# Kernel optimization log

Measured on AMD Instinct MI355X. Metric: run time of the kernel, lower is better.

The kernel has to match this reference:

```python
import jax, jax.numpy as jnp
import numpy as np

TS = 16      # tile size
ST = 4       # stride
IN = 224     # image size
G = (IN - TS) // ST + 1   # 53 tiles per side
L = G * G                 # 2809 tiles
CH = [3 * L, 3 * L // 4, 3 * L // 16, 3 * L // 4, 3 * L]  # [8427,2106,526,2106,8427]

# torch_dct-style unnormalized DCT-II matrix and its exact inverse (DCT-III based)
_n = np.arange(TS)
_k = np.arange(TS)[:, None]
_C = np.cos(np.pi * (2 * _n[None, :] + 1) * _k / (2 * TS))  # [k, n]
D_DCT = jnp.asarray(2.0 * _C, jnp.float32)                   # dct: y = D @ x
_w = np.ones(TS); _w[0] = 0.5
D_IDCT = jnp.asarray((_C.T * _w[None, :]) / TS, jnp.float32) # idct: x = Dinv @ y

# gather/scatter indices for unfold/fold (constants)
IH = (np.arange(G) * ST)[:, None] + np.arange(TS)[None, :]   # [G, TS]
IW = IH


def setup_inputs() -> dict:
    key = jax.random.key(0)
    ks = jax.random.split(key, 9)
    x = jax.random.normal(ks[0], (8, 3, IN, IN), jnp.float32)
    def lin(k, o, c):
        return jax.random.normal(k, (o, c), jnp.float32) * 0.02
    return {
        'x': x,
        'w1': lin(ks[1], CH[1], CH[0]), 'b1': jnp.zeros((CH[1],), jnp.float32),
        'w2': lin(ks[2], CH[2], CH[1]), 'b2': jnp.zeros((CH[2],), jnp.float32),
        'w3': lin(ks[3], CH[3], CH[2]), 'b3': jnp.zeros((CH[3],), jnp.float32),
        'w4': lin(ks[4], CH[4], CH[3]), 'b4': jnp.zeros((CH[4],), jnp.float32),
    }


def _forward(x, w1, b1, w2, b2, w3, b3, w4, b4):
    b = x.shape[0]
    # unfold: gather overlapping 16x16 patches -> [b, 3, G, G, TS, TS]
    p = x[:, :, IH[:, None, :, None], IW[None, :, None, :]]
    # torch ordering after permute+reshape: channel index = l*3 + c
    tiles = p.transpose(0, 2, 3, 1, 4, 5).reshape(b, 3 * L, TS, TS)
    # 2D DCT (unnormalized DCT-II along last two dims)
    dct_tiles = jnp.einsum('km,ln,bcmn->bckl', D_DCT, D_DCT, tiles)
    # mask net: stack of 1x1 convs over the tile-channel dim
    h = dct_tiles / (TS * TS)
    h = jax.nn.relu(jnp.einsum('oc,bchw->bohw', w1, h) + b1[:, None, None])
    h = jax.nn.relu(jnp.einsum('oc,bchw->bohw', w2, h) + b2[:, None, None])
    h = jax.nn.relu(jnp.einsum('oc,bchw->bohw', w3, h) + b3[:, None, None])
    masks = jax.nn.sigmoid(jnp.einsum('oc,bchw->bohw', w4, h) + b4[:, None, None])
    clean_dct = masks * dct_tiles
    # 2D inverse DCT
    clean_tiles = jnp.einsum('mk,nl,bckl->bcmn', D_IDCT, D_IDCT, clean_dct)
    # fold: scatter-add patches back with overlap
    ct = clean_tiles.reshape(b, G, G, 3, TS, TS).transpose(0, 3, 1, 2, 4, 5)
    out = jnp.zeros((b, 3, IN, IN), x.dtype)
    out = out.at[:, :, IH[:, None, :, None], IW[None, :, None, :]].add(ct)
    # scale = fold(unfold(ones)): per-pixel overlap counts (recomputed per call, as in source)
    scale = jnp.zeros((IN, IN), x.dtype)
    scale = scale.at[IH[:, None, :, None], IW[None, :, None, :]].add(
        jnp.ones((G, G, TS, TS), x.dtype))
    return out / scale


def reference(x, w1, b1, w2, b2, w3, b3, w4, b4):
    return _forward(x, w1, b1, w2, b2, w3, b3, w4, b4)
```

## Files before the change

### kernel.cpp

```cpp
#include <hip/hip_runtime.h>
#include <stdint.h>

constexpr int INSZ = 224;
constexpr int GD   = 53;
constexpr int C0R = 8427, C1R = 2106, C2R = 526;
constexpr int C0P = 8448, C1P = 2304, C2P = 640;
constexpr int NTOK = 2048;

typedef __attribute__((ext_vector_type(4))) float f32x4;
typedef __attribute__((ext_vector_type(8))) short bf16x8;

constexpr float CT[64] = {
  1.00000000f,  0.99518473f,  0.98078528f,  0.95694034f,
  0.92387953f,  0.88192126f,  0.83146961f,  0.77301045f,
  0.70710678f,  0.63439328f,  0.55557023f,  0.47139674f,
  0.38268343f,  0.29028468f,  0.19509032f,  0.09801714f,
  0.00000000f, -0.09801714f, -0.19509032f, -0.29028468f,
 -0.38268343f, -0.47139674f, -0.55557023f, -0.63439328f,
 -0.70710678f, -0.77301045f, -0.83146961f, -0.88192126f,
 -0.92387953f, -0.95694034f, -0.98078528f, -0.99518473f,
 -1.00000000f, -0.99518473f, -0.98078528f, -0.95694034f,
 -0.92387953f, -0.88192126f, -0.83146961f, -0.77301045f,
 -0.70710678f, -0.63439328f, -0.55557023f, -0.47139674f,
 -0.38268343f, -0.29028468f, -0.19509032f, -0.09801714f,
 -0.00000000f,  0.09801714f,  0.19509032f,  0.29028468f,
  0.38268343f,  0.47139674f,  0.55557023f,  0.63439328f,
  0.70710678f,  0.77301045f,  0.83146961f,  0.88192126f,
  0.92387953f,  0.95694034f,  0.98078528f,  0.99518473f
};
constexpr float Dfwd(int k, int n) { return 2.0f * CT[((2 * n + 1) * k) & 63]; }
constexpr float Dinv(int n, int k) { return CT[((2 * n + 1) * k) & 63] * (k == 0 ? 0.03125f : 0.0625f); }

constexpr int TRS_R = 20, TRS_T = 336;
constexpr int TRS_SZ = 15 * TRS_T + 15 * TRS_R + 16;

__device__ __forceinline__ unsigned short f2bf(float f) {
  union { float f; unsigned u; } v; v.f = f;
  return (unsigned short)((v.u + 0x7FFFu + ((v.u >> 16) & 1u)) >> 16);
}
__device__ __forceinline__ float bf2f(unsigned short b) {
  union { unsigned u; float f; } v; v.u = ((unsigned)b) << 16;
  return v.f;
}

__device__ __forceinline__ void gload_lds16(const void* g, void* l) {
  __builtin_amdgcn_global_load_lds(
      (__attribute__((address_space(1))) unsigned int*)(uintptr_t)g,
      (__attribute__((address_space(3))) unsigned int*)(unsigned int)(uintptr_t)l,
      16, 0, 0);
}

__device__ __forceinline__ void xcd_tile(int& bx, int& by) {
  const int gx = gridDim.x, gy = gridDim.y;
  const int nwg = gx * gy;
  const int bid = blockIdx.y * gx + blockIdx.x;
  const int cpx = nwg >> 3;
  const int l = (bid & 7) * cpx + (bid >> 3);
  const int stripe = gy << 2;
  const int bxg = l / stripe;
  const int r = l - bxg * stripe;
  const int rem = gx - (bxg << 2);
  const int w = rem < 4 ? rem : 4;
  by = r / w;
  bx = (bxg << 2) + (r - by * w);
}

constexpr int CV1_GPR = C0P / 8;
constexpr int CV1_TOT = C1P * CV1_GPR;
__global__ __launch_bounds__(256)
void cvt_pad8_w1(const float* __restrict__ src, unsigned short* __restrict__ dst) {
  const int i = blockIdx.x * 256 + threadIdx.x;
  if (i >= CV1_TOT) return;
  const int m = i / CV1_GPR;
  const int k0 = (i - m * CV1_GPR) * 8;
  const float* sr = src + (size_t)m * C0R + k0;
  const bool mok = (m < C1R);
  unsigned short h[8];
#pragma unroll
  for (int e = 0; e < 8; ++e)
    h[e] = f2bf((mok && k0 + e < C0R) ? sr[e] : 0.f);
  uint4 pk;
  pk.x = (unsigned)h[0] | ((unsigned)h[1] << 16);
  pk.y = (unsigned)h[2] | ((unsigned)h[3] << 16);
  pk.z = (unsigned)h[4] | ((unsigned)h[5] << 16);
  pk.w = (unsigned)h[6] | ((unsigned)h[7] << 16);
  *(uint4*)&dst[(size_t)m * C0P + k0] = pk;
}

constexpr int CV8_1 = C2P * C1P / 8;
constexpr int CV8_2 = CV8_1 + C1P * C2P / 8;
constexpr int CV8_T = CV8_2 + C0P * C1P / 8;
__global__ __launch_bounds__(256)
void cvt_pad8_all(const float* __restrict__ w2, const float* __restrict__ w3,
                  const float* __restrict__ w4, unsigned short* __restrict__ d2,
                  unsigned short* __restrict__ d3, unsigned short* __restrict__ d4) {
  const int i = blockIdx.x * 256 + threadIdx.x;
  const float* src; unsigned short* dst;
  int m, k0, Kreal, Mreal, Kp;
  if (i < CV8_1) {
    const int gpr = C1P / 8;
    m = i / gpr; k0 = (i - m * gpr) * 8;
    src = w2; dst = d2; Mreal = C2R; Kreal = C1R; Kp = C1P;
  } else if (i < CV8_2) {
    const int j = i - CV8_1;
    const int gpr = C2P / 8;
    m = j / gpr; k0 = (j - m * gpr) * 8;
    src = w3; dst = d3; Mreal = C1R; Kreal = C2R; Kp = C2P;
  } else {
    const int j = i - CV8_2;
    const int gpr = C1P / 8;
    m = j / gpr; k0 = (j - m * gpr) * 8;
    src = w4; dst = d4; Mreal = C0R; Kreal = C1R; Kp = C1P;
  }
  const float* sr = src + (size_t)m * Kreal + k0;
  const bool mok = (m < Mreal);
  unsigned short h[8];
#pragma unroll
  for (int e = 0; e < 8; ++e)
    h[e] = f2bf((mok && k0 + e < Kreal) ? sr[e] : 0.f);
  uint4 pk;
  pk.x = (unsigned)h[0] | ((unsigned)h[1] << 16);
  pk.y = (unsigned)h[2] | ((unsigned)h[3] << 16);
  pk.z = (unsigned)h[4] | ((unsigned)h[5] << 16);
  pk.w = (unsigned)h[6] | ((unsigned)h[7] << 16);
  *(uint4*)&dst[(size_t)m * Kp + k0] = pk;
}

__global__ __launch_bounds__(256)
void dct_h0(const float* __restrict__ x, unsigned short* __restrict__ H0) {
  __shared__ float trp[TRS_SZ];
  __shared__ unsigned short hst[256 * 64];
  const int tid = threadIdx.x;
  const int b   = blockIdx.y;
  const int c0  = blockIdx.x * 64;
  const int t = tid >> 4, q = tid & 15;

  for (int g = 0; g < 4; ++g) {
    const int c = c0 + g * 16 + t;
    float p[16];
    {
      float4 v0{}, v1{}, v2{}, v3{};
      if (c < C0R) {
        const int ch = c % 3, gw = (c / 3) % GD, gh = c / (3 * GD);
        const float* xr = x + ((size_t)(b * 3 + ch) * INSZ + (gh * 4 + q)) * INSZ + gw * 4;
        v0 = *(const float4*)(xr);      v1 = *(const float4*)(xr + 4);
        v2 = *(const float4*)(xr + 8);  v3 = *(const float4*)(xr + 12);
      }
      p[0]=v0.x; p[1]=v0.y; p[2]=v0.z; p[3]=v0.w;
      p[4]=v1.x; p[5]=v1.y; p[6]=v1.z; p[7]=v1.w;
      p[8]=v2.x; p[9]=v2.y; p[10]=v2.z; p[11]=v2.w;
      p[12]=v3.x; p[13]=v3.y; p[14]=v3.z; p[15]=v3.w;
    }
    float r[16];
#pragma unroll
    for (int k = 0; k < 16; ++k) {
      float s = 0.f;
#pragma unroll
      for (int n = 0; n < 16; ++n) s += p[n] * Dfwd(k, n);
      r[k] = s;
    }
    float* wr = &trp[t * TRS_T + q * TRS_R];
#pragma unroll
    for (int k = 0; k < 16; k += 4)
      *(float4*)(wr + k) = make_float4(r[k], r[k+1], r[k+2], r[k+3]);
    __syncthreads();
    const int j = q;
    float rr[16];
#pragma unroll
    for (int i = 0; i < 16; ++i) rr[i] = trp[t * TRS_T + i * TRS_R + j];
#pragma unroll
    for (int k = 0; k < 16; ++k) {
      float s = 0.f;
#pragma unroll
      for (int i = 0; i < 16; ++i) s += rr[i] * Dfwd(k, i);
      hst[(k * 16 + j) * 64 + g * 16 + t] = f2bf(s * (1.f / 256.f));
    }
    __syncthreads();
  }
  const size_t base = ((size_t)b * 256) * C0P + c0;
#pragma unroll
  for (int i = 0; i < 8; ++i) {
    const int s = i * 256 + tid;
    const int kl = s >> 3, c16 = s & 7;
    *(uint4*)&H0[base + (size_t)kl * C0P + c16 * 8] = *(const uint4*)&hst[kl * 64 + c16 * 8];
  }
}

template<int ACT, int OUT_NM, int SPLITK>
__global__ __launch_bounds__(512, 2)
void gemm256(const unsigned short* __restrict__ W, const unsigned short* __restrict__ Ht,
             const float* __restrict__ bias, void* __restrict__ outp,
             int ldo, int Kp, int chunkK) {
  __shared__ unsigned short As[4][8192];
  __shared__ unsigned short Bs[4][8192];
  int bx, by; xcd_tile(bx, by);
  const int m0 = bx * 256, n0 = by * 256;
  const int tid = threadIdx.x;
  const int w = tid >> 6, lane = tid & 63;
  const int wr = w >> 2, wc = w & 3;
  const int lhi = lane >> 4, llo = lane & 15;
  const int kbase = SPLITK ? blockIdx.z * chunkK : 0;
  const int nkt = chunkK >> 5;

  const int srow = tid >> 2;
  const int slgc = ((tid & 3) ^ ((srow >> 1) & 3)) * 8;

  f32x4 acc[8][4];
#pragma unroll
  for (int i = 0; i < 8; ++i)
#pragma unroll
    for (int j = 0; j < 4; ++j) acc[i][j] = f32x4{0.f, 0.f, 0.f, 0.f};

  auto STAGE_A = [&](int kt, int buf) {
    const int kb = kbase + kt * 32 + slgc;
    gload_lds16(W + (size_t)(m0 + srow) * Kp + kb,       &As[buf][w * 512]);
    gload_lds16(W + (size_t)(m0 + 128 + srow) * Kp + kb, &As[buf][4096 + w * 512]);
  };
  auto STAGE_B = [&](int kt, int buf) {
    const int kb = kbase + kt * 32 + slgc;
    gload_lds16(Ht + (size_t)(n0 + srow) * Kp + kb,       &Bs[buf][w * 512]);
    gload_lds16(Ht + (size_t)(n0 + 128 + srow) * Kp + kb, &Bs[buf][4096 + w * 512]);
  };

  STAGE_A(0, 0); STAGE_B(0, 0);
  if (nkt > 1) { STAGE_A(1, 1); STAGE_B(1, 1); }
  if (nkt > 2) { STAGE_A(2, 2); STAGE_B(2, 2); }

  for (int kt = 0; kt < nkt; ++kt) {
    const int buf  = kt & 3;
    const int sbuf = (kt + 3) & 3;
    if (kt + 3 <= nkt)      asm volatile("s_waitcnt vmcnt(8)" ::: "memory");
    else if (kt + 2 == nkt) asm volatile("s_waitcnt vmcnt(4)" ::: "memory");
    else                    asm volatile("s_waitcnt vmcnt(0)" ::: "memory");
    __builtin_amdgcn_s_barrier();
    __builtin_amdgcn_sched_barrier(0);

    bf16x8 af[4], bfr[4];
#pragma unroll
    for (int mi = 0; mi < 4; ++mi) {
      const int row = wr * 128 + mi * 16 + llo;
      af[mi] = *(const bf16x8*)(&As[buf][row * 32 + ((lhi ^ ((row >> 1) & 3)) << 3)]);
    }
#pragma unroll
    for (int ni = 0; ni < 4; ++ni) {
      const int row = wc * 64 + ni * 16 + llo;
      bfr[ni] = *(const bf16x8*)(&Bs[buf][row * 32 + ((lhi ^ ((row >> 1) & 3)) << 3)]);
    }
    if (kt + 3 < nkt) STAGE_A(kt + 3, sbuf);
    __builtin_amdgcn_s_setprio(1);
#pragma unroll
    for (int mi = 0; mi < 4; ++mi)
#pragma unroll
      for (int ni = 0; ni < 4; ++ni)
        acc[mi][ni] = OUT_NM
          ? __builtin_amdgcn_mfma_f32_16x16x32_bf16(bfr[ni], af[mi], acc[mi][ni], 0, 0, 0)
          : __builtin_amdgcn_mfma_f32_16x16x32_bf16(af[mi], bfr[ni], acc[mi][ni], 0, 0, 0);
    __builtin_amdgcn_s_setprio(0);
#pragma unroll
    for (int mi = 0; mi < 4; ++mi) {
      const int row = wr * 128 + 64 + mi * 16 + llo;
      af[mi] = *(const bf16x8*)(&As[buf][row * 32 + ((lhi ^ ((row >> 1) & 3)) << 3)]);
    }
    if (kt + 3 < nkt) STAGE_B(kt + 3, sbuf);
    __builtin_amdgcn_s_setprio(1);
#pragma unroll
    for (int mi = 0; mi < 4; ++mi)
#pragma unroll
      for (int ni = 0; ni < 4; ++ni)
        acc[4 + mi][ni] = OUT_NM
          ? __builtin_amdgcn_mfma_f32_16x16x32_bf16(bfr[ni], af[mi], acc[4 + mi][ni], 0, 0, 0)
          : __builtin_amdgcn_mfma_f32_16x16x32_bf16(af[mi], bfr[ni], acc[4 + mi][ni], 0, 0, 0);
    __builtin_amdgcn_s_setprio(0);
  }

  if (SPLITK) {
    float* pz = (float*)outp + (size_t)blockIdx.z * ((size_t)NTOK * ldo);
#pragma unroll
    for (int mh = 0; mh < 2; ++mh)
#pragma unroll
      for (int mi = 0; mi < 4; ++mi) {
        const int mg = m0 + wr * 128 + mh * 64 + mi * 16 + llo;
#pragma unroll
        for (int ni = 0; ni < 4; ++ni) {
          const int ng = n0 + wc * 64 + ni * 16 + lhi * 4;
#pragma unroll
          for (int r = 0; r < 4; ++r)
            pz[(size_t)(ng + r) * ldo + mg] = acc[mh * 4 + mi][ni][r];
        }
      }
  } else {
    unsigned short* out = (unsigned short*)outp;
#pragma unroll
    for (int mh = 0; mh < 2; ++mh)
#pragma unroll
      for (int mi = 0; mi < 4; ++mi) {
        const int mgb = m0 + wr * 128 + mh * 64 + mi * 16 + lhi * 4;
#pragma unroll
        for (int ni = 0; ni < 4; ++ni) {
          const int ng = n0 + wc * 64 + ni * 16 + llo;
#pragma unroll
          for (int r = 0; r < 4; ++r) {
            const int mg = mgb + r;
            float v = acc[mh * 4 + mi][ni][r] + bias[mg];
            if (ACT == 1) v = fmaxf(v, 0.f);
            else if (ACT == 2) v = 1.f / (1.f + expf(-v));
            out[(size_t)mg * ldo + ng] = f2bf(v);
          }
        }
      }
  }
}

template<int OUT_NM>
__device__ __forceinline__ void gemm_core(
    const unsigned short* __restrict__ W, const unsigned short* __restrict__ Ht,
    unsigned short (*As)[128 * 32], unsigned short (*Bs)[128 * 32],
    int m0, int n0, int Kp, int kbase, int nkt, int w, int lane, f32x4 acc[4][4]) {
  const int wr = w >> 1, wc = w & 1;
  const int lhi = lane >> 4, llo = lane & 15;

  const int chunk0 = w * 64 + lane;
  const int row0 = chunk0 >> 2, kc0 = chunk0 & 3;
  const int kcg0 = kc0 ^ ((row0 >> 1) & 3);
  const int chunk1 = 256 + w * 64 + lane;
  const int row1 = chunk1 >> 2, kc1 = chunk1 & 3;
  const int kcg1 = kc1 ^ ((row1 >> 1) & 3);

  auto STAGE = [&](int kt, int sel) {
    const int kb = kbase + kt * 32;
    gload_lds16(W  + (size_t)(m0 + row0) * Kp + kb + kcg0 * 8, &As[sel][(w * 64) * 8]);
    gload_lds16(Ht + (size_t)(n0 + row0) * Kp + kb + kcg0 * 8, &Bs[sel][(w * 64) * 8]);
    gload_lds16(W  + (size_t)(m0 + row1) * Kp + kb + kcg1 * 8, &As[sel][(256 + w * 64) * 8]);
    gload_lds16(Ht + (size_t)(n0 + row1) * Kp + kb + kcg1 * 8, &Bs[sel][(256 + w * 64) * 8]);
  };

  STAGE(0, 0);
  if (nkt > 1) STAGE(1, 1);

  int cur = 0, nxt = 1, nx2 = 2;
  for (int kt = 0; kt < nkt; ++kt) {
    if (kt + 1 < nkt) {
      asm volatile("s_waitcnt vmcnt(4)" ::: "memory");
      __builtin_amdgcn_s_barrier();
      __builtin_amdgcn_sched_barrier(0);
      if (kt + 2 < nkt) STAGE(kt + 2, nx2);
    } else {
      asm volatile("s_waitcnt vmcnt(0)" ::: "memory");
      __builtin_amdgcn_s_barrier();
      __builtin_amdgcn_sched_barrier(0);
    }
    bf16x8 af[4], bfr[4];
#pragma unroll
    for (int mi = 0; mi < 4; ++mi) {
      const int row = wr * 64 + mi * 16 + llo;
      af[mi] = *(const bf16x8*)(&As[cur][row * 32 + (lhi ^ ((row >> 1) & 3)) * 8]);
    }
#pragma unroll
    for (int ni = 0; ni < 4; ++ni) {
      const int row = wc * 64 + ni * 16 + llo;
      bfr[ni] = *(const bf16x8*)(&Bs[cur][row * 32 + (lhi ^ ((row >> 1) & 3)) * 8]);
    }
#pragma unroll
    for (int mi = 0; mi < 4; ++mi)
#pragma unroll
      for (int ni = 0; ni < 4; ++ni) {
        if (OUT_NM)
          acc[mi][ni] = __builtin_amdgcn_mfma_f32_16x16x32_bf16(bfr[ni], af[mi], acc[mi][ni], 0, 0, 0);
        else
          acc[mi][ni] = __builtin_amdgcn_mfma_f32_16x16x32_bf16(af[mi], bfr[ni], acc[mi][ni], 0, 0, 0);
      }
    const int tmp = cur; cur = nxt; nxt = nx2; nx2 = tmp;
  }
}

__global__ __launch_bounds__(256)
void gemm_splitk(const unsigned short* __restrict__ W, const unsigned short* __restrict__ Ht,
                 float* __restrict__ part, int ldo , int Kp, int chunkK) {
  __shared__ unsigned short As[3][128 * 32];
  __shared__ unsigned short Bs[3][128 * 32];
  int bx, by; xcd_tile(bx, by);
  const int z = blockIdx.z;
  const int tid = threadIdx.x;
  const int w = tid >> 6, lane = tid & 63;
  const int m0 = bx * 128, n0 = by * 128;
  const int wr = w >> 1, wc = w & 1;
  const int lhi = lane >> 4, llo = lane & 15;

  f32x4 acc[4][4];
#pragma unroll
  for (int i = 0; i < 4; ++i)
#pragma unroll
    for (int j = 0; j < 4; ++j) acc[i][j] = f32x4{0.f, 0.f, 0.f, 0.f};

  gemm_core<1>(W, Ht, As, Bs, m0, n0, Kp, z * chunkK, chunkK >> 5, w, lane, acc);

  float* pz = part + (size_t)z * NTOK * ldo;
#pragma unroll
  for (int mi = 0; mi < 4; ++mi) {
    const int mg = m0 + wr * 64 + mi * 16 + llo;
#pragma unroll
    for (int ni = 0; ni < 4; ++ni) {
      const int ng = n0 + wc * 64 + ni * 16 + lhi * 4;
#pragma unroll
      for (int r = 0; r < 4; ++r)
        pz[(size_t)(ng + r) * ldo + mg] = acc[mi][ni][r];
    }
  }
}

__global__ __launch_bounds__(256)
void gemm_splitk_mn(const unsigned short* __restrict__ W, const unsigned short* __restrict__ Ht,
                    float* __restrict__ part, int Kp, int chunkK) {
  __shared__ unsigned short As[3][128 * 32];
  __shared__ unsigned short Bs[3][128 * 32];
  int bx, by; xcd_tile(bx, by);
  const int z = blockIdx.z;
  const int tid = threadIdx.x;
  const int w = tid >> 6, lane = tid & 63;
  const int m0 = bx * 128, n0 = by * 128;
  const int wr = w >> 1, wc = w & 1;
  const int lhi = lane >> 4, llo = lane & 15;
  const int Mloc = gridDim.x * 128;

  f32x4 acc[4][4];
#pragma unroll
  for (int i = 0; i < 4; ++i)
#pragma unroll
    for (int j = 0; j < 4; ++j) acc[i][j] = f32x4{0.f, 0.f, 0.f, 0.f};

  gemm_core<0>(W, Ht, As, Bs, m0, n0, Kp, z * chunkK, chunkK >> 5, w, lane, acc);

  float* pz = part + (size_t)z * Mloc * NTOK;
#pragma unroll
  for (int mi = 0; mi < 4; ++mi) {
    const int mlb = m0 + wr * 64 + mi * 16 + lhi * 4;
#pragma unroll
    for (int ni = 0; ni < 4; ++ni) {
      const int ng = n0 + wc * 64 + ni * 16 + llo;
#pragma unroll
      for (int r = 0; r < 4; ++r)
        pz[(size_t)(mlb + r) * NTOK + ng] = acc[mi][ni][r];
    }
  }
}

__global__ __launch_bounds__(256)
void reduce_sig(const float* __restrict__ part, const float* __restrict__ bias,
                unsigned short* __restrict__ msk, int mbase, int Mloc, int nch) {
  const int i8 = blockIdx.x * 256 + threadIdx.x;
  const int total = Mloc * NTOK / 8;
  if (i8 >= total) return;
  const size_t off = (size_t)i8 * 8;
  const int ml = (int)(off >> 11);
  float s[8] = {0.f, 0.f, 0.f, 0.f, 0.f, 0.f, 0.f, 0.f};
  for (int z = 0; z < nch; ++z) {
    const float4 v0 = *(const float4*)(part + (size_t)z * Mloc * NTOK + off);
    const float4 v1 = *(const float4*)(part + (size_t)z * Mloc * NTOK + off + 4);
    s[0] += v0.x; s[1] += v0.y; s[2] += v0.z; s[3] += v0.w;
    s[4] += v1.x; s[5] += v1.y; s[6] += v1.z; s[7] += v1.w;
  }
  const int mg = mbase + ml;
  const float b = (mg < C0R) ? bias[mg] : 0.f;
  unsigned short h[8];
#pragma unroll
  for (int e = 0; e < 8; ++e)
    h[e] = f2bf(1.f / (1.f + expf(-(s[e] + b))));
  uint4 pk;
  pk.x = (unsigned)h[0] | ((unsigned)h[1] << 16);
  pk.y = (unsigned)h[2] | ((unsigned)h[3] << 16);
  pk.z = (unsigned)h[4] | ((unsigned)h[5] << 16);
  pk.w = (unsigned)h[6] | ((unsigned)h[7] << 16);
  *(uint4*)&msk[(size_t)mg * NTOK + (off & 2047)] = pk;
}

__global__ __launch_bounds__(256)
void reduce_act(const float* __restrict__ part, const float* __restrict__ bias,
                unsigned short* __restrict__ out, int Mp, int Mreal, int nch) {
  const int i8 = blockIdx.x * 256 + threadIdx.x;
  const int total = NTOK * Mp / 8;
  if (i8 >= total) return;
  const size_t off = (size_t)i8 * 8;
  const int m0 = (int)(off % Mp);
  float s[8] = {0.f, 0.f, 0.f, 0.f, 0.f, 0.f, 0.f, 0.f};
  for (int z = 0; z < nch; ++z) {
    const float4 v0 = *(const float4*)(part + (size_t)z * NTOK * Mp + off);
    const float4 v1 = *(const float4*)(part + (size_t)z * NTOK * Mp + off + 4);
    s[0] += v0.x; s[1] += v0.y; s[2] += v0.z; s[3] += v0.w;
    s[4] += v1.x; s[5] += v1.y; s[6] += v1.z; s[7] += v1.w;
  }
  unsigned short h[8];
#pragma unroll
  for (int e = 0; e < 8; ++e) {
    const float b = (m0 + e < Mreal) ? bias[m0 + e] : 0.f;
    h[e] = f2bf(fmaxf(s[e] + b, 0.f));
  }
  uint4 pk;
  pk.x = (unsigned)h[0] | ((unsigned)h[1] << 16);
  pk.y = (unsigned)h[2] | ((unsigned)h[3] << 16);
  pk.z = (unsigned)h[4] | ((unsigned)h[5] << 16);
  pk.w = (unsigned)h[6] | ((unsigned)h[7] << 16);
  *(uint4*)&out[off] = pk;
}

__global__ __launch_bounds__(256)
void mask_idct(const float* __restrict__ x, const unsigned short* __restrict__ masks,
               unsigned short* __restrict__ clean) {
  __shared__ float trp[TRS_SZ];
  const int tid = threadIdx.x;
  const int b   = blockIdx.y;
  const int c0  = blockIdx.x * 16;
  const int t = tid >> 4, q = tid & 15;
  const int c = c0 + t;
  const bool valid = (c < C0R);

  float p[16];
  {
    float4 v0{}, v1{}, v2{}, v3{};
    if (valid) {
      const int ch = c % 3, gw = (c / 3) % GD, gh = c / (3 * GD);
      const float* xr = x + ((size_t)(b * 3 + ch) * INSZ + (gh * 4 + q)) * INSZ + gw * 4;
      v0 = *(const float4*)(xr);      v1 = *(const float4*)(xr + 4);
      v2 = *(const float4*)(xr + 8);  v3 = *(const float4*)(xr + 12);
    }
    p[0]=v0.x; p[1]=v0.y; p[2]=v0.z; p[3]=v0.w;
    p[4]=v1.x; p[5]=v1.y; p[6]=v1.z; p[7]=v1.w;
    p[8]=v2.x; p[9]=v2.y; p[10]=v2.z; p[11]=v2.w;
    p[12]=v3.x; p[13]=v3.y; p[14]=v3.z; p[15]=v3.w;
  }
  float r[16];
#pragma unroll
  for (int k = 0; k < 16; ++k) {
    float s = 0.f;
#pragma unroll
    for (int n = 0; n < 16; ++n) s += p[n] * Dfwd(k, n);
    r[k] = s;
  }
  {
    float* wr = &trp[t * TRS_T + q * TRS_R];
#pragma unroll
    for (int k = 0; k < 16; k += 4)
      *(float4*)(wr + k) = make_float4(r[k], r[k+1], r[k+2], r[k+3]);
  }
  __syncthreads();
  const int j = q;
  float rr[16];
#pragma unroll
  for (int i = 0; i < 16; ++i) rr[i] = trp[t * TRS_T + i * TRS_R + j];
  float cd[16];
  const unsigned short* mrow = masks + (size_t)c * NTOK + (size_t)b * 256 + j;
#pragma unroll
  for (int k = 0; k < 16; ++k) {
    float s = 0.f;
#pragma unroll
    for (int i = 0; i < 16; ++i) s += rr[i] * Dfwd(k, i);
    const float mv = valid ? bf2f(mrow[k * 16]) : 0.f;
    cd[k] = s * mv;
  }
  float t3[16];
#pragma unroll
  for (int m = 0; m < 16; ++m) {
    float s = 0.f;
#pragma unroll
    for (int k = 0; k < 16; ++k) s += cd[k] * Dinv(m, k);
    t3[m] = s;
  }
  __syncthreads();
  {
    float* wr = &trp[t * TRS_T + j * TRS_R];
#pragma unroll
    for (int m = 0; m < 16; m += 4)
      *(float4*)(wr + m) = make_float4(t3[m], t3[m+1], t3[m+2], t3[m+3]);
  }
  __syncthreads();
  float tr[16];
#pragma unroll
  for (int l = 0; l < 16; ++l) tr[l] = trp[t * TRS_T + l * TRS_R + q];
  if (valid) {
    unsigned pk[8];
#pragma unroll
    for (int n2 = 0; n2 < 8; ++n2) {
      float s0 = 0.f, s1 = 0.f;
#pragma unroll
      for (int l = 0; l < 16; ++l) {
        s0 += tr[l] * Dinv(2 * n2, l);
        s1 += tr[l] * Dinv(2 * n2 + 1, l);
      }
      pk[n2] = (unsigned)f2bf(s0) | ((unsigned)f2bf(s1) << 16);
    }
    unsigned short* dst = clean + ((size_t)b * C0R + c) * 256 + q * 16;
    uint4* d4 = (uint4*)dst;
    d4[0] = make_uint4(pk[0], pk[1], pk[2], pk[3]);
    d4[1] = make_uint4(pk[4], pk[5], pk[6], pk[7]);
  }
}

__global__ void overlap_add(const unsigned short* __restrict__ clean, float* __restrict__ out) {
  const int px = blockIdx.x * 256 + threadIdx.x;
  if (px >= 8 * 3 * 224 * 224) return;
  const int j = px % 224;
  const int i = (px / 224) % 224;
  const int bc = px / (224 * 224);
  const int ch = bc % 3, b = bc / 3;
  const int ilo = i - 15;
  const int ghlo = ilo > 0 ? (ilo + 3) >> 2 : 0;
  const int ghhi = (i >> 2) < 52 ? (i >> 2) : 52;
  const int jlo = j - 15;
  const int gwlo = jlo > 0 ? (jlo + 3) >> 2 : 0;
  const int gwhi = (j >> 2) < 52 ? (j >> 2) : 52;
  float sum = 0.f;
  for (int gh = ghlo; gh <= ghhi; ++gh) {
    const int r = i - gh * 4;
    const size_t base = ((size_t)b * C0R + (size_t)gh * (3 * GD) + ch) * 256 + (size_t)r * 16 + j;
    for (int gw = gwlo; gw <= gwhi; ++gw) {
      sum += bf2f(clean[base + (size_t)gw * 764]);
    }
  }
  const int cnt = (ghhi - ghlo + 1) * (gwhi - gwlo + 1);
  out[px] = sum / (float)cnt;
}

extern "C" void kernel_launch(void* const* d_in, const int* in_sizes, int n_in,
                              void* d_out, int out_size, void* d_ws, size_t ws_size,
                              hipStream_t stream) {
  const float* x  = (const float*)d_in[0];
  const float* w1 = (const float*)d_in[1];
  const float* b1 = (const float*)d_in[2];
  const float* w2 = (const float*)d_in[3];
  const float* b2 = (const float*)d_in[4];
  const float* w3 = (const float*)d_in[5];
  const float* b3 = (const float*)d_in[6];
  const float* w4 = (const float*)d_in[7];
  const float* b4 = (const float*)d_in[8];
  float* out = (float*)d_out;
  char* ws = (char*)d_ws;

  const size_t OFF_A = 0;
  const size_t OFF_B = 38928384;
  const size_t OFF_C = 73531392;

  unsigned short* wb1   = (unsigned short*)(ws + OFF_A);
  unsigned short* wb4   = (unsigned short*)(ws + OFF_A);
  unsigned short* clean = (unsigned short*)(ws + OFF_A);

  unsigned short* H0v = (unsigned short*)(ws + OFF_B);
  unsigned short* Y1  = (unsigned short*)(ws + OFF_B);
  unsigned short* wb2 = (unsigned short*)(ws + OFF_B + 9437184);
  unsigned short* wb3 = (unsigned short*)(ws + OFF_B + 12386304);
  unsigned short* Y2  = (unsigned short*)(ws + OFF_B + 15335424);
  unsigned short* msk = (unsigned short*)(ws + OFF_B);

  float* pt1 = (float*)(ws + OFF_C);
  float* pt2 = (float*)(ws + OFF_C);
  float* pt3 = (float*)(ws + OFF_C);
  float* pt4 = (float*)(ws + OFF_C);
  unsigned short* Y3 = (unsigned short*)(ws + OFF_C + 37748736);

  cvt_pad8_w1<<<dim3(CV1_TOT / 256), 256, 0, stream>>>(w1, wb1);
  dct_h0<<<dim3(C0P / 64, 8), 256, 0, stream>>>(x, H0v);

  gemm256<0, 1, 1><<<dim3(C1P / 256, NTOK / 256, 3), 512, 0, stream>>>(
      wb1, H0v, nullptr, pt1, C1P, C0P, 2816);
  reduce_act<<<dim3(NTOK * C1P / 8 / 256), 256, 0, stream>>>(pt1, b1, Y1, C1P, C1R, 3);

  cvt_pad8_all<<<dim3(CV8_T / 256), 256, 0, stream>>>(w2, w3, w4, wb2, wb3, wb4);

  gemm_splitk<<<dim3(C2P / 128, NTOK / 128, 4), 256, 0, stream>>>(wb2, Y1, pt2, C2P, C1P, 576);
  reduce_act<<<dim3(NTOK * C2P / 8 / 256), 256, 0, stream>>>(pt2, b2, Y2, C2P, C2R, 4);

  gemm_splitk<<<dim3(C1P / 128, NTOK / 128, 2), 256, 0, stream>>>(wb3, Y2, pt3, C1P, C2P, 320);
  reduce_act<<<dim3(NTOK * C1P / 8 / 256), 256, 0, stream>>>(pt3, b3, Y3, C1P, C1R, 2);

  gemm256<2, 0, 0><<<dim3(32, NTOK / 256), 512, 0, stream>>>(
      wb4, Y3, b4, msk, NTOK, C1P, C1P);
  gemm_splitk_mn<<<dim3(2, NTOK / 128, 4), 256, 0, stream>>>(
      wb4 + (size_t)8192 * C1P, Y3, pt4, C1P, 576);
  reduce_sig<<<dim3(256 * NTOK / 8 / 256), 256, 0, stream>>>(pt4, b4, msk, 8192, 256, 4);

  mask_idct<<<dim3((C0R + 15) / 16, 8), 256, 0, stream>>>(x, msk, clean);

  overlap_add<<<dim3((8 * 3 * 224 * 224 + 255) / 256), 256, 0, stream>>>(clean, out);
}
```

Measured before the change: 403.3 us.

## Reorder clean-tile layout for coalesced overlap-add and restructure GEMM prefetch

The intermediate clean-tile buffer moves from a per-tile [b, c, 16, 16] layout to a row-major layout indexed by (b, ch, gh, row, gw, col). Adjacent output pixels in overlap_add therefore read nearby addresses instead of addresses spread 764 elements apart. Separately, the GEMM main loop now issues both A and B prefetches right after the barrier and loads both A fragment halves up front, so the MFMA blocks run back to back. This raises register pressure from the extra fragment array.

```diff
diff --git a/kernel.cpp b/kernel.cpp
--- a/kernel.cpp
+++ b/kernel.cpp
@@ -6,6 +6,7 @@
 constexpr int C0R = 8427, C1R = 2106, C2R = 526;
 constexpr int C0P = 8448, C1P = 2304, C2P = 640;
 constexpr int NTOK = 2048;
+constexpr int CROW = GD * 16;
 
 typedef __attribute__((ext_vector_type(4))) float f32x4;
 typedef __attribute__((ext_vector_type(8))) short bf16x8;
@@ -234,42 +235,39 @@
     else                    asm volatile("s_waitcnt vmcnt(0)" ::: "memory");
     __builtin_amdgcn_s_barrier();
     __builtin_amdgcn_sched_barrier(0);
-
-    bf16x8 af[4], bfr[4];
+    if (kt + 3 < nkt) { STAGE_A(kt + 3, sbuf); STAGE_B(kt + 3, sbuf); }
+
+    bf16x8 af0[4], af1[4], bfr[4];
 #pragma unroll
     for (int mi = 0; mi < 4; ++mi) {
       const int row = wr * 128 + mi * 16 + llo;
-      af[mi] = *(const bf16x8*)(&As[buf][row * 32 + ((lhi ^ ((row >> 1) & 3)) << 3)]);
+      af0[mi] = *(const bf16x8*)(&As[buf][row * 32 + ((lhi ^ ((row >> 1) & 3)) << 3)]);
+    }
+#pragma unroll
+    for (int mi = 0; mi < 4; ++mi) {
+      const int row = wr * 128 + 64 + mi * 16 + llo;
+      af1[mi] = *(const bf16x8*)(&As[buf][row * 32 + ((lhi ^ ((row >> 1) & 3)) << 3)]);
     }
 #pragma unroll
     for (int ni = 0; ni < 4; ++ni) {
       const int row = wc * 64 + ni * 16 + llo;
       bfr[ni] = *(const bf16x8*)(&Bs[buf][row * 32 + ((lhi ^ ((row >> 1) & 3)) << 3)]);
     }
-    if (kt + 3 < nkt) STAGE_A(kt + 3, sbuf);
     __builtin_amdgcn_s_setprio(1);
 #pragma unroll
     for (int mi = 0; mi < 4; ++mi)
 #pragma unroll
       for (int ni = 0; ni < 4; ++ni)
         acc[mi][ni] = OUT_NM
-          ? __builtin_amdgcn_mfma_f32_16x16x32_bf16(bfr[ni], af[mi], acc[mi][ni], 0, 0, 0)
-          : __builtin_amdgcn_mfma_f32_16x16x32_bf16(af[mi], bfr[ni], acc[mi][ni], 0, 0, 0);
-    __builtin_amdgcn_s_setprio(0);
-#pragma unroll
-    for (int mi = 0; mi < 4; ++mi) {
-      const int row = wr * 128 + 64 + mi * 16 + llo;
-      af[mi] = *(const bf16x8*)(&As[buf][row * 32 + ((lhi ^ ((row >> 1) & 3)) << 3)]);
-    }
-    if (kt + 3 < nkt) STAGE_B(kt + 3, sbuf);
-    __builtin_amdgcn_s_setprio(1);
+          ? __builtin_amdgcn_mfma_f32_16x16x32_bf16(bfr[ni], af0[mi], acc[mi][ni], 0, 0, 0)
+          : __builtin_amdgcn_mfma_f32_16x16x32_bf16(af0[mi], bfr[ni], acc[mi][ni], 0, 0, 0);
 #pragma unroll
     for (int mi = 0; mi < 4; ++mi)
 #pragma unroll
       for (int ni = 0; ni < 4; ++ni)
         acc[4 + mi][ni] = OUT_NM
-          ? __builtin_amdgcn_mfma_f32_16x16x32_bf16(bfr[ni], af[mi], acc[4 + mi][ni], 0, 0, 0)
-          : __builtin_amdgcn_mfma_f32_16x16x32_bf16(af[mi], bfr[ni], acc[4 + mi][ni], 0, 0, 0);
+          ? __builtin_amdgcn_mfma_f32_16x16x32_bf16(bfr[ni], af1[mi], acc[4 + mi][ni], 0, 0, 0)
+          : __builtin_amdgcn_mfma_f32_16x16x32_bf16(af1[mi], bfr[ni], acc[4 + mi][ni], 0, 0, 0);
     __builtin_amdgcn_s_setprio(0);
   }
 
@@ -512,12 +510,12 @@
   const int t = tid >> 4, q = tid & 15;
   const int c = c0 + t;
   const bool valid = (c < C0R);
+  const int ch = c % 3, gw = (c / 3) % GD, gh = c / (3 * GD);
 
   float p[16];
   {
     float4 v0{}, v1{}, v2{}, v3{};
     if (valid) {
-      const int ch = c % 3, gw = (c / 3) % GD, gh = c / (3 * GD);
       const float* xr = x + ((size_t)(b * 3 + ch) * INSZ + (gh * 4 + q)) * INSZ + gw * 4;
       v0 = *(const float4*)(xr);      v1 = *(const float4*)(xr + 4);
       v2 = *(const float4*)(xr + 8);  v3 = *(const float4*)(xr + 12);
@@ -587,7 +585,8 @@
       }
       pk[n2] = (unsigned)f2bf(s0) | ((unsigned)f2bf(s1) << 16);
     }
-    unsigned short* dst = clean + ((size_t)b * C0R + c) * 256 + q * 16;
+    unsigned short* dst = clean +
+        ((((size_t)(b * 3 + ch) * GD + gh) * 16 + q) * CROW) + gw * 16;
     uint4* d4 = (uint4*)dst;
     d4[0] = make_uint4(pk[0], pk[1], pk[2], pk[3]);
     d4[1] = make_uint4(pk[4], pk[5], pk[6], pk[7]);
@@ -600,7 +599,6 @@
   const int j = px % 224;
   const int i = (px / 224) % 224;
   const int bc = px / (224 * 224);
-  const int ch = bc % 3, b = bc / 3;
   const int ilo = i - 15;
   const int ghlo = ilo > 0 ? (ilo + 3) >> 2 : 0;
   const int ghhi = (i >> 2) < 52 ? (i >> 2) : 52;
@@ -610,10 +608,9 @@
   float sum = 0.f;
   for (int gh = ghlo; gh <= ghhi; ++gh) {
     const int r = i - gh * 4;
-    const size_t base = ((size_t)b * C0R + (size_t)gh * (3 * GD) + ch) * 256 + (size_t)r * 16 + j;
-    for (int gw = gwlo; gw <= gwhi; ++gw) {
-      sum += bf2f(clean[base + (size_t)gw * 764]);
-    }
+    const unsigned short* row = clean + (((size_t)bc * GD + gh) * 16 + r) * CROW;
+    for (int gw = gwlo; gw <= gwhi; ++gw)
+      sum += bf2f(row[j + 12 * gw]);
   }
   const int cnt = (ghhi - ghlo + 1) * (gwhi - gwlo + 1);
   out[px] = sum / (float)cnt;
```

After: 401.2 us. No clear change (-0.5%).
